# Optimization experiments

Hardware: AMD Instinct MI355X
Metric: run time of the kernel (lower is better)

Reference implementation:

```python
import jax, jax.numpy as jnp
import numpy as np

PI = 3.1415926
NPERSEG, HOP = 512, 256
NFRAMES = 17
NFFT_BINS = 257
S = NFFT_BINS * NFRAMES  # 4369
NPATCH = 196
NFREQ = NPATCH // 2 + 1  # 99
D = 128
NF = 2
B = 32
TLEN = 4096

# periodic hann window (scipy default for spectral analysis)
_win_np = (0.5 - 0.5 * np.cos(2.0 * np.pi * np.arange(NPERSEG) / NPERSEG)).astype(np.float32)
WIN = jnp.asarray(_win_np)
WSUM = float(_win_np.sum())  # = 256
_idx_np = np.arange(NFRAMES)[:, None] * HOP + np.arange(NPERSEG)[None, :]
IDX = jnp.asarray(_idx_np)
IDX_FLAT = jnp.asarray(_idx_np.reshape(-1))
OLA_LEN = NPERSEG + (NFRAMES - 1) * HOP  # 4608


def _stft(x):
    # x: (B, D, T) real -> (B, D, 257, 17) complex; matches scipy.signal.stft
    # (window='hann', nperseg=512, noverlap=256, boundary='zeros', 'spectrum' scaling)
    xp = jnp.pad(x, ((0, 0), (0, 0), (HOP, HOP)))
    segs = xp[:, :, IDX] * WIN  # (B, D, 17, 512)
    Z = jnp.fft.rfft(segs, axis=-1) / WSUM
    return jnp.swapaxes(Z, -1, -2)


def _istft(Z):
    # Z: (B, D, 257, 17) complex -> (B, D, 4096) real; matches scipy.signal.istft
    b, d = Z.shape[0], Z.shape[1]
    frames = jnp.fft.irfft(Z, n=NPERSEG, axis=2) * WSUM * WIN[:, None]  # (B, D, 512, 17)
    frames = jnp.swapaxes(frames, 2, 3).reshape(b, d, NFRAMES * NPERSEG)
    ola = jnp.zeros((b, d, OLA_LEN), frames.dtype).at[:, :, IDX_FLAT].add(frames)
    norm = jnp.zeros((OLA_LEN,), frames.dtype).at[IDX_FLAT].add(jnp.tile(WIN * WIN, NFRAMES))
    return (ola / jnp.where(norm > 1e-10, norm, 1.0))[:, :, HOP:-HOP]


def _cx(p):
    return p[..., 0] + 1j * p[..., 1]


def _filter_bank(x, length, fb):
    # x * x / length summed against filter bank with dct-like cosine coefficients
    c = jnp.cos((2.0 * jnp.arange(1, NF + 1, dtype=jnp.float32) - 1.0) * PI / 2.0 * NF)
    fb_eff = jnp.sum(_cx(fb) * c[:, None, None], axis=0)
    return (x * x / length) * fb_eff


def _ln(x, g, b):
    m = x.mean(-1, keepdims=True)
    v = ((x - m) ** 2).mean(-1, keepdims=True)
    return (x - m) / jnp.sqrt(v + 1e-5) * g + b


def _addnorm(x, g1, b1, w1, bb1, w2, bb2, g2, b2):
    x = _ln(x, g1, b1)
    h = jax.nn.gelu(x @ w1 + bb1, approximate=False) @ w2 + bb2 + x
    return _ln(h, g2, b2)


def setup_inputs():
    key = jax.random.key(0)
    ks = jax.random.split(key, 12)
    sc = 0.05
    d = {}
    d["ecg"] = jax.random.normal(ks[0], (B, TLEN, D), jnp.float32)
    d["image"] = jax.random.normal(ks[1], (B, NPATCH, D), jnp.float32)
    d["tfb"] = jax.random.normal(ks[2], (NF, S, D, 2), jnp.float32)
    d["ifb"] = jax.random.normal(ks[3], (NF, NFREQ, D, 2), jnp.float32)
    d["i2t_sel"] = jax.random.normal(ks[4], (NFREQ, D, 2), jnp.float32)
    d["i2t_w"] = jax.random.normal(ks[5], (D, D), jnp.float32) * sc
    d["i2t_b"] = jnp.zeros((D,), jnp.float32)
    d["t_ln1_g"] = jnp.ones((D,), jnp.float32)
    d["t_ln1_b"] = jnp.zeros((D,), jnp.float32)
    d["t_w1"] = jax.random.normal(ks[6], (D, D), jnp.float32) * sc
    d["t_b1"] = jnp.zeros((D,), jnp.float32)
    d["t_w2"] = jax.random.normal(ks[7], (D, D), jnp.float32) * sc
    d["t_b2"] = jnp.zeros((D,), jnp.float32)
    d["t_ln2_g"] = jnp.ones((D,), jnp.float32)
    d["t_ln2_b"] = jnp.zeros((D,), jnp.float32)
    d["i_ln1_g"] = jnp.ones((D,), jnp.float32)
    d["i_ln1_b"] = jnp.zeros((D,), jnp.float32)
    d["i_w1"] = jax.random.normal(ks[8], (D, D), jnp.float32) * sc
    d["i_b1"] = jnp.zeros((D,), jnp.float32)
    d["i_w2"] = jax.random.normal(ks[9], (D, D), jnp.float32) * sc
    d["i_b2"] = jnp.zeros((D,), jnp.float32)
    d["i_ln2_g"] = jnp.ones((D,), jnp.float32)
    d["i_ln2_b"] = jnp.zeros((D,), jnp.float32)
    return d


def reference(ecg, image, tfb, ifb, i2t_sel, i2t_w, i2t_b,
              t_ln1_g, t_ln1_b, t_w1, t_b1, t_w2, t_b2, t_ln2_g, t_ln2_b,
              i_ln1_g, i_ln1_b, i_w1, i_b1, i_w2, i_b2, i_ln2_g, i_ln2_b):
    b, tlen, dm = ecg.shape
    n = image.shape[1]
    Z = _stft(jnp.swapaxes(ecg, 1, 2))  # (B, D, 257, 17)
    z_ecg = jnp.transpose(Z, (0, 2, 3, 1)).reshape(b, S, dm)  # (B, 4369, D) complex
    z_ecg = _filter_bank(z_ecg, S, tfb)
    z_img = jnp.fft.rfft(image, axis=1, norm="ortho")  # (B, 99, D)
    z_img = _filter_bank(z_img, NFREQ, ifb)
    # Image2TextGate: complex select, avg-pool real part over freq bins, 1x1 conv
    g = (z_img * _cx(i2t_sel)).real.mean(axis=1)  # (B, D)
    gate = (jnp.einsum("bd,ed->be", g, i2t_w) + i2t_b)[:, None, :]  # (B, 1, D)
    z_sel = z_ecg * gate
    ecg_t = _istft(jnp.transpose(z_sel.reshape(b, NFFT_BINS, NFRAMES, dm), (0, 3, 1, 2)))
    # torch detaches via numpy roundtrip -> stop_gradient
    ecg_t = jax.lax.stop_gradient(jnp.swapaxes(ecg_t, 1, 2))  # (B, T, D)
    text = _addnorm(ecg_t + ecg, t_ln1_g, t_ln1_b, t_w1, t_b1, t_w2, t_b2, t_ln2_g, t_ln2_b)
    # NOTE: original code discards image_frequency_select output and irffts the
    # filtered _image directly (bug preserved faithfully).
    img_t = jnp.fft.irfft(z_img, n=n, axis=1, norm="ortho")
    img_out = _addnorm(img_t + image, i_ln1_g, i_ln1_b, i_w1, i_b1, i_w2, i_b2, i_ln2_g, i_ln2_b)
    return (text, img_out)
```

## Files before the change

kernel.cpp:

```cpp
#include <hip/hip_runtime.h>
#include <math.h>

#define BB 32
#define DD 128
#define TLEN 4096
#define NSEG 512
#define HOP 256
#define NFR 17
#define NBINS 257
#define STOT 4369
#define NPATCH 196
#define NFREQ 99
#define OLAL 4608

#define FBT2_OFF 0
#define FBT2_SZ  (DD * NFR * NBINS * 2)
#define GBUF_OFF (FBT2_OFF + FBT2_SZ)
#define GATE_OFF (GBUF_OFF + BB * DD)
#define ZI_OFF   (GATE_OFF + BB * DD)
#define ZI_SZ    (BB * NFREQ * DD * 2)
#define X0I_OFF  (ZI_OFF + ZI_SZ)
#define X0I_SZ   (BB * NPATCH * DD)
#define XT_OFF   (X0I_OFF + X0I_SZ)
#define WF_OFF   (XT_OFF + BB * DD * TLEN)

typedef __attribute__((ext_vector_type(8))) short bf16x8;
typedef __attribute__((ext_vector_type(4))) float f32x4;
typedef __attribute__((ext_vector_type(8))) unsigned short u16x8;

__device__ __forceinline__ float gelu_exact(float x) {
    return 0.5f * x * (1.0f + erff(x * 0.70710678118654752f));
}

__device__ __forceinline__ short bf16_rne(float v) {
    unsigned b = __float_as_uint(v);
    return (short)((b + 0x7fffu + ((b >> 16) & 1u)) >> 16);
}

__device__ __forceinline__ void split8(float4 a, float4 b, bf16x8& hi, bf16x8& lo) {
    float v[8] = {a.x, a.y, a.z, a.w, b.x, b.y, b.z, b.w};
#pragma unroll
    for (int e = 0; e < 8; ++e) {
        unsigned bv = __float_as_uint(v[e]);
        unsigned hb = (bv + 0x7fffu + ((bv >> 16) & 1u)) & 0xffff0000u;
        float hf = __uint_as_float(hb);
        hi[e] = (short)(hb >> 16);
        lo[e] = bf16_rne(v[e] - hf);
    }
}

__global__ __launch_bounds__(256) void zero_kernel(float* p, int n) {
    int i = blockIdx.x * 256 + threadIdx.x;
    if (i < n) p[i] = 0.0f;
}

__global__ __launch_bounds__(256) void prep_wfrag(
    const float* __restrict__ w0, const float* __restrict__ w1,
    const float* __restrict__ w2, const float* __restrict__ w3,
    unsigned short* __restrict__ outw) {
    int id = blockIdx.x * 256 + threadIdx.x;
    if (id >= 4 * 2048) return;
    int m = id >> 11;
    int r = id & 2047;
    int kt = r >> 9;
    int n = (r >> 6) & 7;
    int lane = r & 63;
    int k0 = kt * 32 + (lane >> 4) * 8;
    int col = n * 16 + (lane & 15);
    const float* w = (m == 0) ? w0 : (m == 1) ? w1 : (m == 2) ? w2 : w3;
    u16x8 hi, lo;
#pragma unroll
    for (int e = 0; e < 8; ++e) {
        float v = w[(size_t)(k0 + e) * DD + col];
        unsigned bv = __float_as_uint(v);
        unsigned hb = (bv + 0x7fffu + ((bv >> 16) & 1u)) & 0xffff0000u;
        float hf = __uint_as_float(hb);
        float lres = v - hf;
        unsigned bl = __float_as_uint(lres);
        hi[e] = (unsigned short)(hb >> 16);
        lo[e] = (unsigned short)((bl + 0x7fffu + ((bl >> 16) & 1u)) >> 16);
    }
    u16x8* base = (u16x8*)(outw + (size_t)m * 32768);
    base[r] = hi;
    base[2048 + r] = lo;
}

__global__ __launch_bounds__(256) void prep_fb(const float* __restrict__ tfb,
                                               float* __restrict__ fbt2) {
    int idx = blockIdx.x * 256 + threadIdx.x;
    if (idx >= STOT * DD) return;
    int d = idx & 127;
    int s = idx >> 7;
    float2 a = ((const float2*)tfb)[s * DD + d];
    float2 b = ((const float2*)tfb)[STOT * DD + s * DD + d];
    int f = s / NFR, t = s % NFR;
    float2 r;
    r.x = -(a.x + b.x);
    r.y = -(a.y + b.y);
    ((float2*)fbt2)[((size_t)d * NFR + t) * NBINS + f] = r;
}

__global__ __launch_bounds__(256) void transpose_btd(const float* __restrict__ in,
                                                     float* __restrict__ out) {
    __shared__ float tile[32][33];
    int b = blockIdx.z;
    int t0 = blockIdx.x * 32;
    int d0 = blockIdx.y * 32;
    int lx = threadIdx.x;
    int ly = threadIdx.y;
    for (int i = ly; i < 32; i += 8)
        tile[i][lx] = in[((size_t)b * TLEN + t0 + i) * DD + d0 + lx];
    __syncthreads();
    for (int i = ly; i < 32; i += 8)
        out[((size_t)b * DD + d0 + i) * TLEN + t0 + lx] = tile[lx][i];
}

__global__ __launch_bounds__(128) void img_dft(const float* __restrict__ image,
                                               const float* __restrict__ ifb,
                                               const float* __restrict__ sel,
                                               float* __restrict__ zi,
                                               float* __restrict__ gbuf) {
    __shared__ float ctab[NPATCH], stab[NPATCH];
    int b = blockIdx.x / 11;
    int fg = blockIdx.x % 11;
    int d = threadIdx.x;
    for (int m = d; m < NPATCH; m += 128) {
        ctab[m] = cospif(m * (2.0f / 196.0f));
        stab[m] = sinpif(m * (2.0f / 196.0f));
    }
    __syncthreads();
    float accr[9], acci[9];
    int mc[9];
#pragma unroll
    for (int j = 0; j < 9; ++j) { accr[j] = 0.0f; acci[j] = 0.0f; mc[j] = 0; }
    const float* img = image + (size_t)b * NPATCH * DD + d;
    for (int n = 0; n < NPATCH; ++n) {
        float v = img[(size_t)n * DD];
#pragma unroll
        for (int j = 0; j < 9; ++j) {
            float c = ctab[mc[j]], s = stab[mc[j]];
            accr[j] += v * c;
            acci[j] -= v * s;
            mc[j] += fg * 9 + j;
            if (mc[j] >= NPATCH) mc[j] -= NPATCH;
        }
    }
    float gg = 0.0f;
#pragma unroll
    for (int j = 0; j < 9; ++j) {
        int f = fg * 9 + j;
        float Xr = accr[j] * (1.0f / 14.0f);
        float Xi = acci[j] * (1.0f / 14.0f);
        float sr = (Xr * Xr - Xi * Xi) * (1.0f / 99.0f);
        float si = 2.0f * Xr * Xi * (1.0f / 99.0f);
        float2 f0 = ((const float2*)ifb)[f * DD + d];
        float2 f1 = ((const float2*)ifb)[NFREQ * DD + f * DD + d];
        float fbr = -(f0.x + f1.x), fbi = -(f0.y + f1.y);
        float zr = sr * fbr - si * fbi;
        float zm = sr * fbi + si * fbr;
        float2 o; o.x = zr; o.y = zm;
        ((float2*)zi)[((size_t)b * NFREQ + f) * DD + d] = o;
        float2 sl = ((const float2*)sel)[f * DD + d];
        gg += zr * sl.x - zm * sl.y;
    }
    atomicAdd(gbuf + b * DD + d, gg * (1.0f / 99.0f));
}

__global__ __launch_bounds__(128) void gate_kernel(const float* __restrict__ gbuf,
                                                   const float* __restrict__ w,
                                                   const float* __restrict__ bias,
                                                   float* __restrict__ gate) {
    __shared__ float gs[DD];
    int b = blockIdx.x, e = threadIdx.x;
    gs[e] = gbuf[b * DD + e];
    __syncthreads();
    float acc = bias[e];
    const float* wr = w + (size_t)e * DD;
    for (int d = 0; d < DD; ++d) acc += gs[d] * wr[d];
    gate[b * DD + e] = acc;
}

#define SKN 264
#define SK(i) ((i) + ((i) >> 5))

__global__ __launch_bounds__(256, 4) void stft_filter_istft(
    float* xT, const float* __restrict__ fbt2, const float* __restrict__ gate) {
    __shared__ float ar[NFR * SKN];
    __shared__ float ai[NFR * SKN];
    __shared__ float win[NSEG];
    __shared__ float twc[128], tws[128];
    int tid = threadIdx.x;
    int bd = blockIdx.x;
    int d = bd & 127;
    float gat = gate[bd];
    const float scl = gat * (1.0f / 4369.0f);
    float* xrow = xT + (size_t)bd * TLEN;
    const float2* fbrow = (const float2*)(fbt2 + (size_t)d * NFR * NBINS * 2);

    for (int j = tid; j < NSEG; j += 256)
        win[j] = 0.5f - 0.5f * cospif(j * (1.0f / 256.0f));
    if (tid < 128) {
        twc[tid] = cospif(tid * (1.0f / 128.0f));
        tws[tid] = -sinpif(tid * (1.0f / 128.0f));
    }
    __syncthreads();

    for (int t = 0; t < NFR; ++t) {
        int m = tid;
        int src = t * HOP + 2 * m - HOP;
        float e = 0.0f, o = 0.0f;
        if (src >= 0 && src < TLEN) {
            float2 v = *(const float2*)(xrow + src);
            e = v.x; o = v.y;
        }
        e *= win[2 * m]; o *= win[2 * m + 1];
        int r = __brev((unsigned)m) >> 24;
        ar[t * SKN + SK(r)] = e;
        ai[t * SKN + SK(r)] = o;
    }

    for (int s = 1; s <= 8; ++s) {
        __syncthreads();
        int half = 1 << (s - 1);
        for (int j = tid; j < NFR * 128; j += 256) {
            int t = j >> 7, m = j & 127;
            int base = t * SKN;
            int k = m & (half - 1);
            int p = ((m >> (s - 1)) << s) + k;
            int twi = k << (8 - s);
            float c = twc[twi], sn = tws[twi];
            int a0 = base + SK(p), a1 = base + SK(p + half);
            float ur = ar[a0], ui = ai[a0];
            float vr = ar[a1], vi = ai[a1];
            float tr = vr * c - vi * sn;
            float ti = vr * sn + vi * c;
            ar[a0] = ur + tr; ai[a0] = ui + ti;
            ar[a1] = ur - tr; ai[a1] = ui - ti;
        }
    }
    __syncthreads();

    float y1r[9], y1i[9], y2r[9], y2i[9];
#pragma unroll
    for (int it = 0; it < 9; ++it) {
        int j = tid + it * 256;
        if (j < NFR * 129) {
            int t = j / 129, m = j - t * 129;
            int base = t * SKN;
            const float2* fbr = fbrow + t * NBINS;
            if (m == 0) {
                float re = ar[base + SK(0)], im = ai[base + SK(0)];
                float z0 = (re + im) * (1.0f / 256.0f);
                float zN = (re - im) * (1.0f / 256.0f);
                float2 fb0 = fbr[0], fbN = fbr[256];
                y1r[it] = z0 * z0 * fb0.x * scl; y1i[it] = 0.0f;
                y2r[it] = zN * zN * fbN.x * scl; y2i[it] = 0.0f;
            } else if (m == 128) {
                float Zr = ar[base + SK(128)], Zi = ai[base + SK(128)];
                float zr = Zr * (1.0f / 256.0f), zi2 = -Zi * (1.0f / 256.0f);
                float sr = zr * zr - zi2 * zi2, si = 2.0f * zr * zi2;
                float2 fb = fbr[128];
                y1r[it] = (sr * fb.x - si * fb.y) * scl;
                y1i[it] = (sr * fb.y + si * fb.x) * scl;
                y2r[it] = 0.0f; y2i[it] = 0.0f;
            } else {
                float Amr = ar[base + SK(m)],       Ami = ai[base + SK(m)];
                float Acr = ar[base + SK(256 - m)], Aci = ai[base + SK(256 - m)];
                float c = cospif(m * (1.0f / 256.0f));
                float sn = sinpif(m * (1.0f / 256.0f));
                {
                    float Br = Acr, Bi = -Aci;
                    float xer = 0.5f * (Amr + Br), xei = 0.5f * (Ami + Bi);
                    float xo_r = 0.5f * (Ami - Bi), xo_i = -0.5f * (Amr - Br);
                    float Xr = xer + c * xo_r + sn * xo_i;
                    float Xi = xei + c * xo_i - sn * xo_r;
                    float zr = Xr * (1.0f / 256.0f), zi2 = Xi * (1.0f / 256.0f);
                    float sr = zr * zr - zi2 * zi2, si = 2.0f * zr * zi2;
                    float2 fb = fbr[m];
                    y1r[it] = (sr * fb.x - si * fb.y) * scl;
                    y1i[it] = (sr * fb.y + si * fb.x) * scl;
                }
                {
                    float Br = Amr, Bi = -Ami;
                    float xer = 0.5f * (Acr + Br), xei = 0.5f * (Aci + Bi);
                    float xo_r = 0.5f * (Aci - Bi), xo_i = -0.5f * (Acr - Br);
                    float Xr = xer - c * xo_r + sn * xo_i;
                    float Xi = xei - c * xo_i - sn * xo_r;
                    float zr = Xr * (1.0f / 256.0f), zi2 = Xi * (1.0f / 256.0f);
                    float sr = zr * zr - zi2 * zi2, si = 2.0f * zr * zi2;
                    float2 fb = fbr[256 - m];
                    y2r[it] = (sr * fb.x - si * fb.y) * scl;
                    y2i[it] = (sr * fb.y + si * fb.x) * scl;
                }
            }
        }
    }
    __syncthreads();

#pragma unroll
    for (int it = 0; it < 9; ++it) {
        int j = tid + it * 256;
        if (j < NFR * 129) {
            int t = j / 129, m = j - t * 129;
            int base = t * SKN;
            if (m == 0) {
                float Er = 0.5f * (y1r[it] + y2r[it]);
                float Dr = 0.5f * (y1r[it] - y2r[it]);
                ar[base + SK(0)] = Er;
                ai[base + SK(0)] = -Dr;
            } else if (m == 128) {
                ar[base + SK(1)] = y1r[it];
                ai[base + SK(1)] = y1i[it];
            } else {
                float c = cospif(m * (1.0f / 256.0f));
                float sn = sinpif(m * (1.0f / 256.0f));
                float Er = 0.5f * (y1r[it] + y2r[it]);
                float Ei = 0.5f * (y1i[it] - y2i[it]);
                float Dr = 0.5f * (y1r[it] - y2r[it]);
                float Di = 0.5f * (y1i[it] + y2i[it]);
                float Or = Dr * c - Di * sn;
                float Oi = Dr * sn + Di * c;
                int r1 = __brev((unsigned)m) >> 24;
                ar[base + SK(r1)] = Er - Oi;
                ai[base + SK(r1)] = -(Ei + Or);
                int r2 = __brev((unsigned)(256 - m)) >> 24;
                ar[base + SK(r2)] = Er + Oi;
                ai[base + SK(r2)] = Ei - Or;
            }
        }
    }

    for (int s = 1; s <= 8; ++s) {
        __syncthreads();
        int half = 1 << (s - 1);
        for (int j = tid; j < NFR * 128; j += 256) {
            int t = j >> 7, m = j & 127;
            int base = t * SKN;
            int k = m & (half - 1);
            int p = ((m >> (s - 1)) << s) + k;
            int twi = k << (8 - s);
            float c = twc[twi], sn = tws[twi];
            int a0 = base + SK(p), a1 = base + SK(p + half);
            float ur = ar[a0], ui = ai[a0];
            float vr = ar[a1], vi = ai[a1];
            float tr = vr * c - vi * sn;
            float ti = vr * sn + vi * c;
            ar[a0] = ur + tr; ai[a0] = ui + ti;
            ar[a1] = ur - tr; ai[a1] = ui - ti;
        }
    }
    __syncthreads();

    for (int j = tid; j < TLEN; j += 256) {
        int p = j + HOP;
        int t1 = p >> 8;
        int t0 = t1 - 1;
        int i1 = p & 255;
        int i0 = i1 + 256;
        int h1 = t1 * SKN + SK(i1 >> 1);
        int h0 = t0 * SKN + SK(i0 >> 1);
        float v1, v0;
        if (j & 1) { v1 = -ai[h1]; v0 = -ai[h0]; }
        else       { v1 =  ar[h1]; v0 =  ar[h0]; }
        float s = v0 * win[i0] + v1 * win[i1];
        float s2 = win[i1];
        float c2 = 1.0f - s2;
        xrow[j] = s / (s2 * s2 + c2 * c2);
    }
}

__global__ __launch_bounds__(128) void img_irfft(const float* __restrict__ zi,
                                                 const float* __restrict__ image,
                                                 float* __restrict__ x0img) {
    __shared__ float ctab[NPATCH], stab[NPATCH];
    int b = blockIdx.x / 14;
    int ng = blockIdx.x % 14;
    int d = threadIdx.x;
    for (int m = d; m < NPATCH; m += 128) {
        ctab[m] = cospif(m * (2.0f / 196.0f));
        stab[m] = sinpif(m * (2.0f / 196.0f));
    }
    __syncthreads();
    const float2* zrow = (const float2*)zi + (size_t)b * NFREQ * DD + d;
    float acc[14];
    int mc[14];
    float2 z0 = zrow[0];
#pragma unroll
    for (int j = 0; j < 14; ++j) { acc[j] = z0.x; mc[j] = 0; }
    for (int f = 1; f <= 97; ++f) {
        float2 z = zrow[(size_t)f * DD];
#pragma unroll
        for (int j = 0; j < 14; ++j) {
            int n = ng * 14 + j;
            mc[j] += n;
            if (mc[j] >= NPATCH) mc[j] -= NPATCH;
            acc[j] += 2.0f * (z.x * ctab[mc[j]] - z.y * stab[mc[j]]);
        }
    }
    float2 z98 = zrow[98 * (size_t)DD];
#pragma unroll
    for (int j = 0; j < 14; ++j) {
        int n = ng * 14 + j;
        float a = acc[j] + ((n & 1) ? -z98.x : z98.x);
        float y = a * (1.0f / 14.0f);
        size_t idx = ((size_t)b * NPATCH + n) * DD + d;
        x0img[idx] = y + image[idx];
    }
}

#define XLNS 132

__device__ __forceinline__ void mlp_gemm(const float* __restrict__ ax,
                                         const unsigned short* __restrict__ wf,
                                         int lane, f32x4 acc[8]) {
#pragma unroll
    for (int n = 0; n < 8; ++n) acc[n] = (f32x4){0.f, 0.f, 0.f, 0.f};
    const bf16x8* bh0 = (const bf16x8*)wf;
    const bf16x8* bl0 = (const bf16x8*)(wf + 16384);
#pragma unroll 1
    for (int kt = 0; kt < 4; ++kt) {
        float4 va = *(const float4*)(ax + kt * 32);
        float4 vb = *(const float4*)(ax + kt * 32 + 4);
        bf16x8 ahi, alo;
        split8(va, vb, ahi, alo);
        const bf16x8* bh = bh0 + kt * 512 + lane;
        const bf16x8* bl = bl0 + kt * 512 + lane;
#pragma unroll
        for (int n = 0; n < 8; ++n) {
            bf16x8 wh = bh[n * 64];
            bf16x8 wl = bl[n * 64];
            acc[n] = __builtin_amdgcn_mfma_f32_16x16x32_bf16(ahi, wh, acc[n], 0, 0, 0);
            acc[n] = __builtin_amdgcn_mfma_f32_16x16x32_bf16(alo, wh, acc[n], 0, 0, 0);
            acc[n] = __builtin_amdgcn_mfma_f32_16x16x32_bf16(ahi, wl, acc[n], 0, 0, 0);
        }
    }
}

template <int FUSED>
__global__ __launch_bounds__(256) void addnorm_kernel(
    const float* __restrict__ srcA, const float* __restrict__ srcB,
    const float* __restrict__ ln1g, const float* __restrict__ ln1b,
    const unsigned short* __restrict__ w1f, const float* __restrict__ b1,
    const unsigned short* __restrict__ w2f, const float* __restrict__ b2,
    const float* __restrict__ ln2g, const float* __restrict__ ln2b,
    float* __restrict__ out) {
    __shared__ __align__(16) float xln[64 * XLNS];
    int tid = threadIdx.x;
    int b = 0, t0 = 0;
    size_t R0 = 0;
    if (FUSED) {
        b = blockIdx.x >> 6;
        t0 = (blockIdx.x & 63) * 64;
        for (int i = tid; i < 64 * 128; i += 256) {
            int dd = i >> 6, r = i & 63;
            xln[r * XLNS + dd] = srcA[((size_t)b * DD + dd) * TLEN + t0 + r];
        }
        __syncthreads();
        for (int i = tid; i < 64 * 128; i += 256) {
            int r = i >> 7, dd = i & 127;
            xln[r * XLNS + dd] += srcB[((size_t)b * TLEN + t0 + r) * DD + dd];
        }
    } else {
        R0 = (size_t)blockIdx.x * 64;
        for (int i = tid; i < 64 * 128; i += 256) {
            int r = i >> 7, dd = i & 127;
            xln[r * XLNS + dd] = srcA[(R0 + r) * DD + dd];
        }
    }
    __syncthreads();
    int wave = tid >> 6, lane = tid & 63;
    for (int r = wave; r < 64; r += 4) {
        float v0 = xln[r * XLNS + lane];
        float v1 = xln[r * XLNS + 64 + lane];
        float s = v0 + v1, ss = v0 * v0 + v1 * v1;
        for (int off = 32; off > 0; off >>= 1) {
            s += __shfl_xor(s, off);
            ss += __shfl_xor(ss, off);
        }
        float mean = s * (1.0f / 128.0f);
        float var = ss * (1.0f / 128.0f) - mean * mean;
        float rstd = rsqrtf(var + 1e-5f);
        xln[r * XLNS + lane] = (v0 - mean) * rstd * ln1g[lane] + ln1b[lane];
        xln[r * XLNS + 64 + lane] = (v1 - mean) * rstd * ln1g[64 + lane] + ln1b[64 + lane];
    }
    __syncthreads();
    int q = lane >> 4, c = lane & 15;
    int rbase = wave * 16 + q * 4;
    const float* ax = &xln[(wave * 16 + c) * XLNS + q * 8];
    f32x4 acc[8];
    mlp_gemm(ax, w1f, lane, acc);
    float res[8][4];
#pragma unroll
    for (int n = 0; n < 8; ++n)
#pragma unroll
        for (int r = 0; r < 4; ++r)
            res[n][r] = xln[(rbase + r) * XLNS + n * 16 + c];
#pragma unroll
    for (int n = 0; n < 8; ++n) {
        float bb = b1[n * 16 + c];
#pragma unroll
        for (int r = 0; r < 4; ++r)
            acc[n][r] = gelu_exact(acc[n][r] + bb);
    }
    __syncthreads();
#pragma unroll
    for (int n = 0; n < 8; ++n)
#pragma unroll
        for (int r = 0; r < 4; ++r)
            xln[(rbase + r) * XLNS + n * 16 + c] = acc[n][r];
    __syncthreads();
    mlp_gemm(ax, w2f, lane, acc);
#pragma unroll
    for (int n = 0; n < 8; ++n) {
        float bb = b2[n * 16 + c];
#pragma unroll
        for (int r = 0; r < 4; ++r)
            acc[n][r] += bb + res[n][r];
    }
    float s4[4] = {0.f, 0.f, 0.f, 0.f}, ss4[4] = {0.f, 0.f, 0.f, 0.f};
#pragma unroll
    for (int n = 0; n < 8; ++n)
#pragma unroll
        for (int r = 0; r < 4; ++r) {
            float h = acc[n][r];
            s4[r] += h; ss4[r] += h * h;
        }
#pragma unroll
    for (int off = 8; off > 0; off >>= 1) {
#pragma unroll
        for (int r = 0; r < 4; ++r) {
            s4[r] += __shfl_xor(s4[r], off);
            ss4[r] += __shfl_xor(ss4[r], off);
        }
    }
    float g2v[8], b2v[8];
#pragma unroll
    for (int n = 0; n < 8; ++n) {
        g2v[n] = ln2g[n * 16 + c];
        b2v[n] = ln2b[n * 16 + c];
    }
#pragma unroll
    for (int r = 0; r < 4; ++r) {
        float mean = s4[r] * (1.0f / 128.0f);
        float var = ss4[r] * (1.0f / 128.0f) - mean * mean;
        float rstd = rsqrtf(var + 1e-5f);
        size_t orow = FUSED ? ((size_t)b * TLEN + t0 + rbase + r) * DD
                            : (R0 + rbase + r) * DD;
#pragma unroll
        for (int n = 0; n < 8; ++n)
            out[orow + n * 16 + c] = (acc[n][r] - mean) * rstd * g2v[n] + b2v[n];
    }
}

extern "C" void kernel_launch(void* const* d_in, const int* in_sizes, int n_in,
                              void* d_out, int out_size, void* d_ws, size_t ws_size,
                              hipStream_t stream) {
    (void)in_sizes; (void)n_in; (void)out_size; (void)ws_size;
    const float* ecg   = (const float*)d_in[0];
    const float* image = (const float*)d_in[1];
    const float* tfb   = (const float*)d_in[2];
    const float* ifb   = (const float*)d_in[3];
    const float* sel   = (const float*)d_in[4];
    const float* i2t_w = (const float*)d_in[5];
    const float* i2t_b = (const float*)d_in[6];
    const float* t_ln1_g = (const float*)d_in[7];
    const float* t_ln1_b = (const float*)d_in[8];
    const float* t_w1 = (const float*)d_in[9];
    const float* t_b1 = (const float*)d_in[10];
    const float* t_w2 = (const float*)d_in[11];
    const float* t_b2 = (const float*)d_in[12];
    const float* t_ln2_g = (const float*)d_in[13];
    const float* t_ln2_b = (const float*)d_in[14];
    const float* i_ln1_g = (const float*)d_in[15];
    const float* i_ln1_b = (const float*)d_in[16];
    const float* i_w1 = (const float*)d_in[17];
    const float* i_b1 = (const float*)d_in[18];
    const float* i_w2 = (const float*)d_in[19];
    const float* i_b2 = (const float*)d_in[20];
    const float* i_ln2_g = (const float*)d_in[21];
    const float* i_ln2_b = (const float*)d_in[22];
    float* out = (float*)d_out;
    float* ws = (float*)d_ws;
    unsigned short* wfb = (unsigned short*)(ws + WF_OFF);

    zero_kernel<<<16, 256, 0, stream>>>(ws + GBUF_OFF, BB * DD);
    prep_wfrag<<<32, 256, 0, stream>>>(t_w1, t_w2, i_w1, i_w2, wfb);
    prep_fb<<<(STOT * DD + 255) / 256, 256, 0, stream>>>(tfb, ws + FBT2_OFF);
    {
        dim3 tb(32, 8);
        dim3 tg(TLEN / 32, DD / 32, BB);
        transpose_btd<<<tg, tb, 0, stream>>>(ecg, ws + XT_OFF);
    }
    img_dft<<<BB * 11, 128, 0, stream>>>(image, ifb, sel, ws + ZI_OFF, ws + GBUF_OFF);
    gate_kernel<<<BB, 128, 0, stream>>>(ws + GBUF_OFF, i2t_w, i2t_b, ws + GATE_OFF);
    stft_filter_istft<<<BB * DD, 256, 0, stream>>>(ws + XT_OFF, ws + FBT2_OFF, ws + GATE_OFF);
    addnorm_kernel<1><<<BB * (TLEN / 64), 256, 0, stream>>>(
        ws + XT_OFF, ecg, t_ln1_g, t_ln1_b, wfb + 0, t_b1, wfb + 32768, t_b2,
        t_ln2_g, t_ln2_b, out);
    img_irfft<<<BB * 14, 128, 0, stream>>>(ws + ZI_OFF, image, ws + X0I_OFF);
    addnorm_kernel<0><<<(BB * NPATCH) / 64, 256, 0, stream>>>(
        ws + X0I_OFF, nullptr, i_ln1_g, i_ln1_b, wfb + 65536, i_b1, wfb + 98304, i_b2,
        i_ln2_g, i_ln2_b, out + (size_t)BB * TLEN * DD);
}
```

Measured before the change: 633.8 us.

## Replace shared-memory radix-2 FFT stages with register/shuffle wave-level 256-point FFT

Each 256-point complex FFT (forward STFT and inverse) is now done by one wavefront holding four points per lane in registers. It runs a DIF radix-4 first stage and then cross-lane butterflies via __shfl_xor, replacing eight barrier-separated LDS butterfly stages. Spectra are stored as float2 with an XOR swizzle instead of padded split arrays, and the OLA normalization divide is replaced by a precomputed reciprocal table. This removes many __syncthreads and LDS round-trips in exchange for more register pressure and shuffle traffic.

```diff
diff --git a/kernel.cpp b/kernel.cpp
--- a/kernel.cpp
+++ b/kernel.cpp
@@ -180,16 +180,33 @@
     gate[b * DD + e] = acc;
 }
 
-#define SKN 264
-#define SK(i) ((i) + ((i) >> 5))
+#define SWZ(e) ((e) ^ (((e) >> 4) & 15))
+
+#define CMULW(dr, di, c, s, xr, xi) { float _t = (dr)*(c) - (di)*(s); xi = (dr)*(s) + (di)*(c); xr = _t; }
+#define BF(xr, xi, h) { \
+    float pr_ = __shfl_xor(xr, h), pi_ = __shfl_xor(xi, h); \
+    float dr2_ = fmaf(sg##h, xr, pr_), di2_ = fmaf(sg##h, xi, pi_); \
+    CMULW(dr2_, di2_, tc##h, ts##h, xr, xi) }
+#define SSTG(h) BF(a0r, a0i, h) BF(a1r, a1i, h) BF(a2r, a2i, h) BF(a3r, a3i, h)
+#define BF1(xr, xi) { \
+    float pr_ = __shfl_xor(xr, 1), pi_ = __shfl_xor(xi, 1); \
+    xr = fmaf(sg1, xr, pr_); xi = fmaf(sg1, xi, pi_); }
+#define DIF256() { \
+    float dr_, di_; \
+    dr_ = a0r - a2r; di_ = a0i - a2i; a0r += a2r; a0i += a2i; CMULW(dr_, di_, wa_c, wa_s, a2r, a2i) \
+    dr_ = a1r - a3r; di_ = a1i - a3i; a1r += a3r; a1i += a3i; CMULW(dr_, di_, wb_c, wb_s, a3r, a3i) \
+    dr_ = a0r - a1r; di_ = a0i - a1i; a0r += a1r; a0i += a1i; CMULW(dr_, di_, wc_c, wc_s, a1r, a1i) \
+    dr_ = a2r - a3r; di_ = a2i - a3i; a2r += a3r; a2i += a3i; CMULW(dr_, di_, wc_c, wc_s, a3r, a3i) \
+    SSTG(32) SSTG(16) SSTG(8) SSTG(4) SSTG(2) \
+    BF1(a0r, a0i) BF1(a1r, a1i) BF1(a2r, a2i) BF1(a3r, a3i) }
 
 __global__ __launch_bounds__(256, 4) void stft_filter_istft(
     float* xT, const float* __restrict__ fbt2, const float* __restrict__ gate) {
-    __shared__ float ar[NFR * SKN];
-    __shared__ float ai[NFR * SKN];
+    __shared__ float2 spec[NFR * 256];
     __shared__ float win[NSEG];
-    __shared__ float twc[128], tws[128];
+    __shared__ float rnorm[256];
     int tid = threadIdx.x;
+    int lane = tid & 63, wave = tid >> 6;
     int bd = blockIdx.x;
     int d = bd & 127;
     float gat = gate[bd];
@@ -199,44 +216,52 @@
 
     for (int j = tid; j < NSEG; j += 256)
         win[j] = 0.5f - 0.5f * cospif(j * (1.0f / 256.0f));
-    if (tid < 128) {
-        twc[tid] = cospif(tid * (1.0f / 128.0f));
-        tws[tid] = -sinpif(tid * (1.0f / 128.0f));
-    }
-    __syncthreads();
-
-    for (int t = 0; t < NFR; ++t) {
-        int m = tid;
-        int src = t * HOP + 2 * m - HOP;
-        float e = 0.0f, o = 0.0f;
-        if (src >= 0 && src < TLEN) {
-            float2 v = *(const float2*)(xrow + src);
-            e = v.x; o = v.y;
-        }
-        e *= win[2 * m]; o *= win[2 * m + 1];
-        int r = __brev((unsigned)m) >> 24;
-        ar[t * SKN + SK(r)] = e;
-        ai[t * SKN + SK(r)] = o;
-    }
-
-    for (int s = 1; s <= 8; ++s) {
-        __syncthreads();
-        int half = 1 << (s - 1);
-        for (int j = tid; j < NFR * 128; j += 256) {
-            int t = j >> 7, m = j & 127;
-            int base = t * SKN;
-            int k = m & (half - 1);
-            int p = ((m >> (s - 1)) << s) + k;
-            int twi = k << (8 - s);
-            float c = twc[twi], sn = tws[twi];
-            int a0 = base + SK(p), a1 = base + SK(p + half);
-            float ur = ar[a0], ui = ai[a0];
-            float vr = ar[a1], vi = ai[a1];
-            float tr = vr * c - vi * sn;
-            float ti = vr * sn + vi * c;
-            ar[a0] = ur + tr; ai[a0] = ui + ti;
-            ar[a1] = ur - tr; ai[a1] = ui - ti;
-        }
+    {
+        float s2 = 0.5f - 0.5f * cospif(tid * (1.0f / 256.0f));
+        float c2 = 1.0f - s2;
+        rnorm[tid] = 1.0f / (s2 * s2 + c2 * c2);
+    }
+
+    float wa_c = cospif(lane * (1.0f / 128.0f)), wa_s = -sinpif(lane * (1.0f / 128.0f));
+    float wb_c = cospif((64 + lane) * (1.0f / 128.0f)), wb_s = -sinpif((64 + lane) * (1.0f / 128.0f));
+    float wc_c = cospif(lane * (1.0f / 64.0f)),  wc_s = -sinpif(lane * (1.0f / 64.0f));
+#define MKT(h) \
+    float tc##h, ts##h, sg##h; \
+    { int set_ = lane & h; float ang_ = (float)(lane & (h - 1)) * (1.0f / h); \
+      tc##h = set_ ? cospif(ang_) : 1.0f; \
+      ts##h = set_ ? -sinpif(ang_) : 0.0f; \
+      sg##h = set_ ? -1.0f : 1.0f; }
+    MKT(32) MKT(16) MKT(8) MKT(4) MKT(2)
+    float sg1 = (lane & 1) ? -1.0f : 1.0f;
+#undef MKT
+
+    int eS[4], eL[4];
+#pragma unroll
+    for (int j = 0; j < 4; ++j) {
+        int i = j * 64 + lane;
+        eS[j] = SWZ((int)(__brev((unsigned)i) >> 24));
+        eL[j] = SWZ(i);
+    }
+    __syncthreads();
+
+    for (int t = wave; t < NFR; t += 4) {
+        float a0r, a0i, a1r, a1i, a2r, a2i, a3r, a3i;
+#define LOADJ(j, xr, xi) { \
+        int i_ = (j) * 64 + lane; \
+        int src_ = t * HOP + 2 * i_ - HOP; \
+        float er_ = 0.0f, oi_ = 0.0f; \
+        if (src_ >= 0 && src_ < TLEN) { \
+            float2 v_ = *(const float2*)(xrow + src_); er_ = v_.x; oi_ = v_.y; } \
+        float2 w_ = *(const float2*)(win + 2 * i_); \
+        xr = er_ * w_.x; xi = oi_ * w_.y; }
+        LOADJ(0, a0r, a0i) LOADJ(1, a1r, a1i) LOADJ(2, a2r, a2i) LOADJ(3, a3r, a3i)
+#undef LOADJ
+        DIF256()
+        float2* sp = spec + t * 256;
+        sp[eS[0]] = make_float2(a0r, a0i);
+        sp[eS[1]] = make_float2(a1r, a1i);
+        sp[eS[2]] = make_float2(a2r, a2i);
+        sp[eS[3]] = make_float2(a3r, a3i);
     }
     __syncthreads();
 
@@ -246,17 +271,19 @@
         int j = tid + it * 256;
         if (j < NFR * 129) {
             int t = j / 129, m = j - t * 129;
-            int base = t * SKN;
+            const float2* sp = spec + t * 256;
             const float2* fbr = fbrow + t * NBINS;
             if (m == 0) {
-                float re = ar[base + SK(0)], im = ai[base + SK(0)];
+                float2 v = sp[0];
+                float re = v.x, im = v.y;
                 float z0 = (re + im) * (1.0f / 256.0f);
                 float zN = (re - im) * (1.0f / 256.0f);
                 float2 fb0 = fbr[0], fbN = fbr[256];
                 y1r[it] = z0 * z0 * fb0.x * scl; y1i[it] = 0.0f;
                 y2r[it] = zN * zN * fbN.x * scl; y2i[it] = 0.0f;
             } else if (m == 128) {
-                float Zr = ar[base + SK(128)], Zi = ai[base + SK(128)];
+                float2 v = sp[SWZ(128)];
+                float Zr = v.x, Zi = v.y;
                 float zr = Zr * (1.0f / 256.0f), zi2 = -Zi * (1.0f / 256.0f);
                 float sr = zr * zr - zi2 * zi2, si = 2.0f * zr * zi2;
                 float2 fb = fbr[128];
@@ -264,8 +291,10 @@
                 y1i[it] = (sr * fb.y + si * fb.x) * scl;
                 y2r[it] = 0.0f; y2i[it] = 0.0f;
             } else {
-                float Amr = ar[base + SK(m)],       Ami = ai[base + SK(m)];
-                float Acr = ar[base + SK(256 - m)], Aci = ai[base + SK(256 - m)];
+                float2 vm = sp[SWZ(m)];
+                float2 vc = sp[SWZ(256 - m)];
+                float Amr = vm.x, Ami = vm.y;
+                float Acr = vc.x, Aci = vc.y;
                 float c = cospif(m * (1.0f / 256.0f));
                 float sn = sinpif(m * (1.0f / 256.0f));
                 {
@@ -302,15 +331,13 @@
         int j = tid + it * 256;
         if (j < NFR * 129) {
             int t = j / 129, m = j - t * 129;
-            int base = t * SKN;
+            float2* sp = spec + t * 256;
             if (m == 0) {
                 float Er = 0.5f * (y1r[it] + y2r[it]);
                 float Dr = 0.5f * (y1r[it] - y2r[it]);
-                ar[base + SK(0)] = Er;
-                ai[base + SK(0)] = -Dr;
+                sp[0] = make_float2(Er, -Dr);
             } else if (m == 128) {
-                ar[base + SK(1)] = y1r[it];
-                ai[base + SK(1)] = y1i[it];
+                sp[SWZ(128)] = make_float2(y1r[it], y1i[it]);
             } else {
                 float c = cospif(m * (1.0f / 256.0f));
                 float sn = sinpif(m * (1.0f / 256.0f));
@@ -320,52 +347,37 @@
                 float Di = 0.5f * (y1i[it] + y2i[it]);
                 float Or = Dr * c - Di * sn;
                 float Oi = Dr * sn + Di * c;
-                int r1 = __brev((unsigned)m) >> 24;
-                ar[base + SK(r1)] = Er - Oi;
-                ai[base + SK(r1)] = -(Ei + Or);
-                int r2 = __brev((unsigned)(256 - m)) >> 24;
-                ar[base + SK(r2)] = Er + Oi;
-                ai[base + SK(r2)] = Ei - Or;
+                sp[SWZ(m)] = make_float2(Er - Oi, -(Ei + Or));
+                sp[SWZ(256 - m)] = make_float2(Er + Oi, Ei - Or);
             }
         }
     }
-
-    for (int s = 1; s <= 8; ++s) {
-        __syncthreads();
-        int half = 1 << (s - 1);
-        for (int j = tid; j < NFR * 128; j += 256) {
-            int t = j >> 7, m = j & 127;
-            int base = t * SKN;
-            int k = m & (half - 1);
-            int p = ((m >> (s - 1)) << s) + k;
-            int twi = k << (8 - s);
-            float c = twc[twi], sn = tws[twi];
-            int a0 = base + SK(p), a1 = base + SK(p + half);
-            float ur = ar[a0], ui = ai[a0];
-            float vr = ar[a1], vi = ai[a1];
-            float tr = vr * c - vi * sn;
-            float ti = vr * sn + vi * c;
-            ar[a0] = ur + tr; ai[a0] = ui + ti;
-            ar[a1] = ur - tr; ai[a1] = ui - ti;
-        }
-    }
-    __syncthreads();
-
+    __syncthreads();
+
+    for (int t = wave; t < NFR; t += 4) {
+        float2* sp = spec + t * 256;
+        float2 v0 = sp[eL[0]], v1 = sp[eL[1]], v2 = sp[eL[2]], v3 = sp[eL[3]];
+        float a0r = v0.x, a0i = v0.y, a1r = v1.x, a1i = v1.y;
+        float a2r = v2.x, a2i = v2.y, a3r = v3.x, a3i = v3.y;
+        DIF256()
+        sp[eS[0]] = make_float2(a0r, a0i);
+        sp[eS[1]] = make_float2(a1r, a1i);
+        sp[eS[2]] = make_float2(a2r, a2i);
+        sp[eS[3]] = make_float2(a3r, a3i);
+    }
+    __syncthreads();
+
+    const float* specf = (const float*)spec;
     for (int j = tid; j < TLEN; j += 256) {
         int p = j + HOP;
-        int t1 = p >> 8;
-        int t0 = t1 - 1;
-        int i1 = p & 255;
-        int i0 = i1 + 256;
-        int h1 = t1 * SKN + SK(i1 >> 1);
-        int h0 = t0 * SKN + SK(i0 >> 1);
-        float v1, v0;
-        if (j & 1) { v1 = -ai[h1]; v0 = -ai[h0]; }
-        else       { v1 =  ar[h1]; v0 =  ar[h0]; }
+        int t1 = p >> 8, t0 = t1 - 1;
+        int i1 = p & 255, i0 = i1 + 256;
+        int comp = j & 1;
+        float v1 = specf[(t1 * 256 + SWZ(i1 >> 1)) * 2 + comp];
+        float v0 = specf[(t0 * 256 + SWZ(i0 >> 1)) * 2 + comp];
+        if (comp) { v1 = -v1; v0 = -v0; }
         float s = v0 * win[i0] + v1 * win[i1];
-        float s2 = win[i1];
-        float c2 = 1.0f - s2;
-        xrow[j] = s / (s2 * s2 + c2 * c2);
+        xrow[j] = s * rnorm[i1];
     }
 }
 
```

Result: slower. 675.2 us (+6.5%).
